# Kernel tuning notes

Measured on AMD Instinct MI355X. Metric: run time of the kernel, lower is better.

Reference implementation:

```python
import jax, jax.numpy as jnp
import numpy as np

N_HEAD = 16
DIM_K = 64
DIM_MODEL = N_HEAD * DIM_K  # 1024; seq_len is forced to equal dim_model by the reshape
SCALE = float(DIM_K ** 0.5)


def setup_inputs() -> dict:
    key = jax.random.key(0)
    ks = jax.random.split(key, 4)
    B, S, D = 32, DIM_MODEL, 1024
    x = jax.random.normal(ks[0], (B, S, D), dtype=jnp.float32)
    glorot = float(1.0 / np.sqrt(D))
    Wq = jax.random.normal(ks[1], (D, DIM_MODEL), dtype=jnp.float32) * glorot
    Wk = jax.random.normal(ks[2], (D, DIM_MODEL), dtype=jnp.float32) * glorot
    Wv = jax.random.normal(ks[3], (D, DIM_MODEL), dtype=jnp.float32) * glorot
    bq = jnp.zeros((DIM_MODEL,), jnp.float32)
    bk = jnp.zeros((DIM_MODEL,), jnp.float32)
    bv = jnp.zeros((DIM_MODEL,), jnp.float32)
    return {"x": x, "Wq": Wq, "bq": bq, "Wk": Wk, "bk": bk, "Wv": Wv, "bv": bv}


def reference(x, Wq, bq, Wk, bk, Wv, bv):
    # x: [B, S, D] with S == DIM_MODEL (required by the original reshape)
    B = x.shape[0]
    q = x @ Wq + bq  # [B, S, dm]
    k = x @ Wk + bk
    v = x @ Wv + bv
    # TF1 K.batch_dot(q, k, axes=[-1,-1]) -> tf.matmul(q, k, adjoint_a=True):
    # contracts over the SEQUENCE axis -> [B, dm, dm]
    y = jnp.einsum('bsd,bse->bde', q, k) / SCALE
    # softmax over dim_k-sized chunks of the last axis
    y = y.reshape(B, DIM_MODEL, N_HEAD, DIM_K)
    y = jax.nn.softmax(y, axis=-1)
    y = y.reshape(B, DIM_MODEL, DIM_MODEL)
    # TF1 K.batch_dot(v, y, axes=[2,3]) -> tf.matmul(v, y) (no adjoints)
    out = jnp.einsum('bsd,bde->bse', v, y)  # [B, S, dm]
    return out
```

## Files before the change

### kernel.cpp

```cpp
#include <hip/hip_runtime.h>
#include <hip/hip_bf16.h>

#define DM 1024
#define NB 32

typedef __bf16 bf16_t;
typedef __attribute__((ext_vector_type(8))) __bf16 bf16x8;
typedef __attribute__((ext_vector_type(4))) float  f32x4;

typedef __attribute__((address_space(1))) void gas_void;
typedef __attribute__((address_space(3))) void las_void;

__device__ __forceinline__ void async_lds16(const bf16_t* g, bf16_t* l) {
    __builtin_amdgcn_global_load_lds((gas_void*)g, (las_void*)l, 16, 0, 0);
}

__device__ inline float bf2f(bf16_t v) {
    union { unsigned short s; __bf16 b; } u; u.b = v;
    union { unsigned int i; float f; } w; w.i = ((unsigned int)u.s) << 16;
    return w.f;
}
__device__ inline bf16_t f2bf(float f) {
    union { unsigned int i; float f; } w; w.f = f;
    unsigned int r = (w.i + 0x7FFFu + ((w.i >> 16) & 1u)) >> 16;
    union { unsigned short s; __bf16 b; } u; u.s = (unsigned short)r;
    return u.b;
}

enum EpiMode { EPI_NONE = 0, EPI_BIAS_ROW = 1, EPI_BIAS_COL = 2, EPI_SCALE = 3 };

__global__ void detect_mode(const unsigned short* __restrict__ x, int* __restrict__ mode)
{
    if (threadIdx.x == 0 && blockIdx.x == 0) {
        int hits = 0;
        for (int i = 0; i < 2048; ++i) {
            unsigned e = (x[i] >> 7) & 0xFFu;
            hits += (e >= 0x8Du) ? 1 : 0;
        }
        *mode = (hits >= 16) ? 1 : 0;
    }
}

__global__ void convert_x(const void* __restrict__ xin, bf16_t* __restrict__ xb,
                          const int* __restrict__ modep, long long off, long long n8)
{
    const long long i = (long long)blockIdx.x * blockDim.x + threadIdx.x;
    if (i >= n8) return;
    bf16x8 o;
    if (*modep) {
        const float* s = (const float*)xin + off + i * 8;
#pragma unroll
        for (int j = 0; j < 8; ++j) o[j] = f2bf(s[j]);
    } else {
        o = *(const bf16x8*)((const bf16_t*)xin + off + i * 8);
    }
    *(bf16x8*)(xb + i * 8) = o;
}

__global__ void transpose3(const void* __restrict__ Wq, const void* __restrict__ Wk,
                           const void* __restrict__ Wv, bf16_t* __restrict__ Wt,
                           const int* __restrict__ modep)
{
    const int md = *modep;
    const void* src = (blockIdx.z == 0) ? Wq : (blockIdx.z == 1) ? Wk : Wv;
    bf16_t* dst = Wt + (size_t)blockIdx.z * DM * DM;
    __shared__ bf16_t T[64][72];
    const int tid = threadIdx.x;
    const int r  = tid >> 2;
    const int cp = tid & 3;
    const int r0 = blockIdx.y * 64;
    const int c0 = blockIdx.x * 64;
    const size_t base = (size_t)(r0 + r) * DM + c0 + cp * 16;
    bf16_t tmp[16];
    if (md) {
        const float* s = (const float*)src + base;
#pragma unroll
        for (int j = 0; j < 16; ++j) tmp[j] = f2bf(s[j]);
    } else {
        const bf16_t* s = (const bf16_t*)src + base;
        bf16x8 a = *(const bf16x8*)s;
        bf16x8 b = *(const bf16x8*)(s + 8);
#pragma unroll
        for (int j = 0; j < 8; ++j) { tmp[j] = a[j]; tmp[8 + j] = b[j]; }
    }
#pragma unroll
    for (int j = 0; j < 16; ++j) T[cp * 16 + j][r] = tmp[j];
    __syncthreads();
    bf16_t* d = dst + (size_t)(c0 + r) * DM + r0 + cp * 16;
    bf16x8 w0, w1;
#pragma unroll
    for (int j = 0; j < 8; ++j) w0[j] = T[r][cp * 16 + j];
#pragma unroll
    for (int j = 0; j < 8; ++j) w1[j] = T[r][cp * 16 + 8 + j];
    *(bf16x8*)d = w0;
    *(bf16x8*)(d + 8) = w1;
}

template <int MODE, bool DUALOUT>
__global__ __launch_bounds__(512, 2)
void gemm_nt8(const bf16_t* __restrict__ A, long long sA,
              const bf16_t* __restrict__ B, long long sB,
              void* __restrict__ C, long long sC, long long cOff,
              const void* __restrict__ bias, const int* __restrict__ modep,
              float scale)
{
    constexpr int K = 1024;
    constexpr int NT = K / 64;
    extern __shared__ bf16_t L[];

    int bx, by, z;
    {
        const int nwg  = 16 * (int)gridDim.z;
        const int orig = (int)blockIdx.x + 4 * ((int)blockIdx.y + 4 * (int)blockIdx.z);
        const int nid  = (orig & 7) * (nwg >> 3) + (orig >> 3);
        bx = nid & 3; by = (nid >> 2) & 3; z = nid >> 4;
    }

    const bf16_t* Ab = A + (size_t)z * (size_t)sA;
    const bf16_t* Bb = B + (size_t)z * (size_t)sB;
    const int gm0 = by * 256, gn0 = bx * 256;

    const int tid  = threadIdx.x;
    const int lane = tid & 63;
    const int w    = tid >> 6;
    const int rb   = w >> 1;
    const int cb   = w & 1;
    const int lm   = lane & 15;
    const int kg   = lane >> 4;

    f32x4 acc[4][2][4];
#pragma unroll
    for (int p = 0; p < 4; ++p)
#pragma unroll
        for (int i = 0; i < 2; ++i)
#pragma unroll
            for (int j = 0; j < 4; ++j) acc[p][i][j] = (f32x4)0.0f;

    auto stage = [&](int kt, int s, int b) {
        const bf16_t* P  = (s == 0 || s == 3) ? Ab : Bb;
        const int     g0 = (s == 0 || s == 3) ? gm0 : gn0;
        const int     h  = (s >= 2) ? 1 : 0;
        bf16_t* dst = L + (b * 4 + s) * 8192;
#pragma unroll
        for (int i = 0; i < 2; ++i) {
            const int ci  = i * 512 + tid;
            const int row = ci >> 3;
            const int kc  = (ci & 7) ^ (row & 7);
            async_lds16(P + (size_t)(g0 + h * 128 + row) * K + kt * 64 + kc * 8,
                        dst + ci * 8);
        }
    };

    auto rdfrag = [&](int b, int s, int r, int kc) -> bf16x8 {
        const int byte = r * 128 + ((kc ^ (r & 7)) * 16);
        return *(const bf16x8*)((const char*)(L + (b * 4 + s) * 8192) + byte);
    };

#pragma unroll
    for (int s = 0; s < 4; ++s) stage(0, s, 0);
    asm volatile("s_waitcnt vmcnt(2)" ::: "memory");
    __builtin_amdgcn_s_barrier();

#pragma unroll 1
    for (int kt = 0; kt < NT; ++kt) {
        const int cur = kt & 1;
        const int nkt = (kt + 1 < NT) ? kt + 1 : 0;
#pragma unroll
        for (int p = 0; p < 4; ++p) {
            const int sA_ = (p >> 1) ? 3 : 0;
            const int sB_ = (p & 1) ? 2 : 1;
            bf16x8 af[2][2], bg[4][2];
#pragma unroll
            for (int mt = 0; mt < 2; ++mt)
#pragma unroll
                for (int kk = 0; kk < 2; ++kk)
                    af[mt][kk] = rdfrag(cur, sA_, rb * 32 + mt * 16 + lm, kk * 4 + kg);
#pragma unroll
            for (int nt = 0; nt < 4; ++nt)
#pragma unroll
                for (int kk = 0; kk < 2; ++kk)
                    bg[nt][kk] = rdfrag(cur, sB_, cb * 64 + nt * 16 + lm, kk * 4 + kg);
            stage(nkt, p, cur ^ 1);
            __builtin_amdgcn_s_barrier();
            asm volatile("s_waitcnt lgkmcnt(0)" ::: "memory");
            __builtin_amdgcn_sched_barrier(0);
            __builtin_amdgcn_s_setprio(1);
#pragma unroll
            for (int kk = 0; kk < 2; ++kk)
#pragma unroll
                for (int mt = 0; mt < 2; ++mt)
#pragma unroll
                    for (int nt = 0; nt < 4; ++nt)
                        acc[p][mt][nt] = __builtin_amdgcn_mfma_f32_16x16x32_bf16(
                            af[mt][kk], bg[nt][kk], acc[p][mt][nt], 0, 0, 0);
            __builtin_amdgcn_s_setprio(0);
            if (p == 1) { asm volatile("s_waitcnt vmcnt(4)" ::: "memory"); }
            if (p == 3) { asm volatile("s_waitcnt vmcnt(2)" ::: "memory"); }
            __builtin_amdgcn_s_barrier();
        }
    }

    const int md = *modep;
#pragma unroll
    for (int p = 0; p < 4; ++p) {
        const int rbase = gm0 + (p >> 1) * 128 + rb * 32;
        const int cbase = gn0 + (p & 1) * 128 + cb * 64;
#pragma unroll
        for (int mt = 0; mt < 2; ++mt) {
            float rbias[4];
            if (MODE == EPI_BIAS_ROW) {
#pragma unroll
                for (int r = 0; r < 4; ++r) {
                    const int i = rbase + mt * 16 + kg * 4 + r;
                    rbias[r] = md ? ((const float*)bias)[i] : bf2f(((const bf16_t*)bias)[i]);
                }
            }
#pragma unroll
            for (int nt = 0; nt < 4; ++nt) {
                const int col = cbase + nt * 16 + lm;
                float cbias = 0.f;
                if (MODE == EPI_BIAS_COL)
                    cbias = md ? ((const float*)bias)[col] : bf2f(((const bf16_t*)bias)[col]);
#pragma unroll
                for (int r = 0; r < 4; ++r) {
                    const int row = rbase + mt * 16 + kg * 4 + r;
                    float vv = acc[p][mt][nt][r];
                    if (MODE == EPI_BIAS_ROW) vv += rbias[r];
                    if (MODE == EPI_BIAS_COL) vv += cbias;
                    if (MODE == EPI_SCALE)    vv *= scale;
                    const size_t off = (size_t)cOff + (size_t)z * sC + (size_t)row * 1024 + col;
                    if (DUALOUT && md) ((float*)C)[off] = vv;
                    else               ((bf16_t*)C)[off] = f2bf(vv);
                }
            }
        }
    }
}

__global__ void softmax_t_inplace(bf16_t* __restrict__ Y)
{
    const int b = blockIdx.z;
    int idx = blockIdx.x;
    int I = 0;
    while (idx >= 16 - I) { idx -= 16 - I; ++I; }
    const int J = I + idx;

    const int tid = threadIdx.x;
    const int r  = tid >> 2;
    const int cp = tid & 3;

    bf16_t* base = Y + ((size_t)b << 20);
    bf16_t* t0 = base + (size_t)(I * 64 + r) * DM + J * 64 + cp * 16;
    bf16_t* t1 = base + (size_t)(J * 64 + r) * DM + I * 64 + cp * 16;

    __shared__ bf16_t P0[64][72];
    __shared__ bf16_t P1[64][72];

    bf16x8 a0 = *(const bf16x8*)t0;
    bf16x8 a1 = *(const bf16x8*)(t0 + 8);
    bf16x8 c0v, c1v;
    if (J != I) { c0v = *(const bf16x8*)t1; c1v = *(const bf16x8*)(t1 + 8); }

    {
        float f[16];
#pragma unroll
        for (int j = 0; j < 8; ++j) f[j] = bf2f(a0[j]);
#pragma unroll
        for (int j = 0; j < 8; ++j) f[8 + j] = bf2f(a1[j]);
        float m = -1e30f;
#pragma unroll
        for (int j = 0; j < 16; ++j) m = fmaxf(m, f[j]);
        m = fmaxf(m, __shfl_xor(m, 1));
        m = fmaxf(m, __shfl_xor(m, 2));
        float s = 0.f;
#pragma unroll
        for (int j = 0; j < 16; ++j) { f[j] = __expf(f[j] - m); s += f[j]; }
        s += __shfl_xor(s, 1);
        s += __shfl_xor(s, 2);
        const float inv = 1.0f / s;
#pragma unroll
        for (int j = 0; j < 16; ++j) P0[cp * 16 + j][r] = f2bf(f[j] * inv);
    }
    if (J != I) {
        float f[16];
#pragma unroll
        for (int j = 0; j < 8; ++j) f[j] = bf2f(c0v[j]);
#pragma unroll
        for (int j = 0; j < 8; ++j) f[8 + j] = bf2f(c1v[j]);
        float m = -1e30f;
#pragma unroll
        for (int j = 0; j < 16; ++j) m = fmaxf(m, f[j]);
        m = fmaxf(m, __shfl_xor(m, 1));
        m = fmaxf(m, __shfl_xor(m, 2));
        float s = 0.f;
#pragma unroll
        for (int j = 0; j < 16; ++j) { f[j] = __expf(f[j] - m); s += f[j]; }
        s += __shfl_xor(s, 1);
        s += __shfl_xor(s, 2);
        const float inv = 1.0f / s;
#pragma unroll
        for (int j = 0; j < 16; ++j) P1[cp * 16 + j][r] = f2bf(f[j] * inv);
    }
    __syncthreads();

    bf16x8 w0, w1;
#pragma unroll
    for (int j = 0; j < 8; ++j) w0[j] = P0[r][cp * 16 + j];
#pragma unroll
    for (int j = 0; j < 8; ++j) w1[j] = P0[r][cp * 16 + 8 + j];
    *(bf16x8*)t1 = w0;
    *(bf16x8*)(t1 + 8) = w1;
    if (J != I) {
#pragma unroll
        for (int j = 0; j < 8; ++j) w0[j] = P1[r][cp * 16 + j];
#pragma unroll
        for (int j = 0; j < 8; ++j) w1[j] = P1[r][cp * 16 + 8 + j];
        *(bf16x8*)t0 = w0;
        *(bf16x8*)(t0 + 8) = w1;
    }
}

extern "C" void kernel_launch(void* const* d_in, const int* in_sizes, int n_in,
                              void* d_out, int out_size, void* d_ws, size_t ws_size,
                              hipStream_t stream)
{
    const void* x  = d_in[0];
    const void* Wq = d_in[1];
    const void* bq = d_in[2];
    const void* Wk = d_in[3];
    const void* bk = d_in[4];
    const void* Wv = d_in[5];
    const void* bv = d_in[6];

    static bool attr_done = false;
    if (!attr_done) {
        hipFuncSetAttribute((const void*)gemm_nt8<EPI_BIAS_ROW, false>,
                            hipFuncAttributeMaxDynamicSharedMemorySize, 131072);
        hipFuncSetAttribute((const void*)gemm_nt8<EPI_BIAS_COL, false>,
                            hipFuncAttributeMaxDynamicSharedMemorySize, 131072);
        hipFuncSetAttribute((const void*)gemm_nt8<EPI_SCALE, false>,
                            hipFuncAttributeMaxDynamicSharedMemorySize, 131072);
        hipFuncSetAttribute((const void*)gemm_nt8<EPI_NONE, true>,
                            hipFuncAttributeMaxDynamicSharedMemorySize, 131072);
        attr_done = true;
    }

    char* ws = (char*)d_ws;
    int* mode = (int*)ws;
    const size_t MB2 = (size_t)DM * DM * 2;
    const size_t hdr = 256;
    int CB = NB;
    while (CB > 1 && hdr + 3 * MB2 + 4 * (size_t)CB * MB2 > ws_size) CB >>= 1;

    bf16_t* Wt = (bf16_t*)(ws + hdr);
    bf16_t* xb = (bf16_t*)(ws + hdr + 3 * MB2);
    bf16_t* qt = xb + (size_t)CB * DM * DM;
    bf16_t* kt = qt + (size_t)CB * DM * DM;
    bf16_t* y  = kt + (size_t)CB * DM * DM;
    bf16_t* v  = qt;

    detect_mode<<<1, 64, 0, stream>>>((const unsigned short*)x, mode);
    transpose3<<<dim3(16, 16, 3), 256, 0, stream>>>(Wq, Wk, Wv, Wt, mode);

    const long long msz = (long long)DM * DM;
    for (int c = 0; c < NB; c += CB) {
        const int zb = (NB - c < CB) ? (NB - c) : CB;
        const long long n8 = (long long)zb * msz / 8;
        convert_x<<<(int)((n8 + 255) / 256), 256, 0, stream>>>(x, xb, mode, (long long)c * msz, n8);

        const dim3 g8(4, 4, zb), blk8(512);
        gemm_nt8<EPI_BIAS_ROW, false><<<g8, blk8, 131072, stream>>>(Wt, 0, xb, msz, qt, msz, 0, bq, mode, 1.f);
        gemm_nt8<EPI_BIAS_ROW, false><<<g8, blk8, 131072, stream>>>(Wt + msz, 0, xb, msz, kt, msz, 0, bk, mode, 1.f);
        gemm_nt8<EPI_SCALE, false><<<g8, blk8, 131072, stream>>>(qt, msz, kt, msz, y, msz, 0, nullptr, mode, 0.125f);
        softmax_t_inplace<<<dim3(136, 1, zb), 256, 0, stream>>>(y);
        gemm_nt8<EPI_BIAS_COL, false><<<g8, blk8, 131072, stream>>>(xb, msz, Wt + 2 * msz, 0, v, msz, 0, bv, mode, 1.f);
        gemm_nt8<EPI_NONE, true><<<g8, blk8, 131072, stream>>>(v, msz, y, msz, d_out, msz, (long long)c * msz, nullptr, mode, 1.f);
    }
}
```

Before: 698.7 us.

## Software-pipeline LDS fragment reads with double-buffered registers across MFMA phases

Restructures the GEMM main loop so LDS fragment reads for the next phase are issued before the current phase's MFMAs, using two register sets for the A and B fragments. The stage layout is reordered so A and B halves alternate, and phase order changes so fragments are reused across two consecutive phases. Barriers and vmcnt waits are rearranged to match. The goal is to hide LDS latency behind matrix math, at the cost of more VGPRs and a more fragile wait/barrier schedule.

Result: faster. 671.2 us (-3.9%).

```diff
diff --git a/kernel.cpp b/kernel.cpp
--- a/kernel.cpp
+++ b/kernel.cpp
@@ -136,9 +136,11 @@
 #pragma unroll
             for (int j = 0; j < 4; ++j) acc[p][i][j] = (f32x4)0.0f;
 
+    bf16x8 af0[2][2], af1[2][2], bg0[4][2], bg1[4][2];
+
     auto stage = [&](int kt, int s, int b) {
-        const bf16_t* P  = (s == 0 || s == 3) ? Ab : Bb;
-        const int     g0 = (s == 0 || s == 3) ? gm0 : gn0;
+        const bf16_t* P  = (s & 1) ? Bb : Ab;
+        const int     g0 = (s & 1) ? gn0 : gm0;
         const int     h  = (s >= 2) ? 1 : 0;
         bf16_t* dst = L + (b * 4 + s) * 8192;
 #pragma unroll
@@ -155,56 +157,86 @@
         const int byte = r * 128 + ((kc ^ (r & 7)) * 16);
         return *(const bf16x8*)((const char*)(L + (b * 4 + s) * 8192) + byte);
     };
+    auto rdA = [&](int b, int s, bf16x8 (&dst)[2][2]) {
+#pragma unroll
+        for (int mt = 0; mt < 2; ++mt)
+#pragma unroll
+            for (int kk = 0; kk < 2; ++kk)
+                dst[mt][kk] = rdfrag(b, s, rb * 32 + mt * 16 + lm, kk * 4 + kg);
+    };
+    auto rdB = [&](int b, int s, bf16x8 (&dst)[4][2]) {
+#pragma unroll
+        for (int nt = 0; nt < 4; ++nt)
+#pragma unroll
+            for (int kk = 0; kk < 2; ++kk)
+                dst[nt][kk] = rdfrag(b, s, cb * 64 + nt * 16 + lm, kk * 4 + kg);
+    };
+
+#define MFMA_PHASE(P, AF, BG)                                                  \
+    __builtin_amdgcn_s_setprio(1);                                             \
+    _Pragma("unroll")                                                          \
+    for (int kk = 0; kk < 2; ++kk)                                             \
+        _Pragma("unroll")                                                      \
+        for (int mt = 0; mt < 2; ++mt)                                         \
+            _Pragma("unroll")                                                  \
+            for (int nt = 0; nt < 4; ++nt)                                     \
+                acc[P][mt][nt] = __builtin_amdgcn_mfma_f32_16x16x32_bf16(      \
+                    AF[mt][kk], BG[nt][kk], acc[P][mt][nt], 0, 0, 0);          \
+    __builtin_amdgcn_s_setprio(0);
 
 #pragma unroll
     for (int s = 0; s < 4; ++s) stage(0, s, 0);
+    asm volatile("s_waitcnt vmcnt(4)" ::: "memory");
+    __builtin_amdgcn_s_barrier();
+    rdA(0, 0, af0);
+    rdB(0, 1, bg0);
     asm volatile("s_waitcnt vmcnt(2)" ::: "memory");
     __builtin_amdgcn_s_barrier();
 
 #pragma unroll 1
     for (int kt = 0; kt < NT; ++kt) {
         const int cur = kt & 1;
+        const int nxt = cur ^ 1;
         const int nkt = (kt + 1 < NT) ? kt + 1 : 0;
-#pragma unroll
-        for (int p = 0; p < 4; ++p) {
-            const int sA_ = (p >> 1) ? 3 : 0;
-            const int sB_ = (p & 1) ? 2 : 1;
-            bf16x8 af[2][2], bg[4][2];
-#pragma unroll
-            for (int mt = 0; mt < 2; ++mt)
-#pragma unroll
-                for (int kk = 0; kk < 2; ++kk)
-                    af[mt][kk] = rdfrag(cur, sA_, rb * 32 + mt * 16 + lm, kk * 4 + kg);
-#pragma unroll
-            for (int nt = 0; nt < 4; ++nt)
-#pragma unroll
-                for (int kk = 0; kk < 2; ++kk)
-                    bg[nt][kk] = rdfrag(cur, sB_, cb * 64 + nt * 16 + lm, kk * 4 + kg);
-            stage(nkt, p, cur ^ 1);
-            __builtin_amdgcn_s_barrier();
-            asm volatile("s_waitcnt lgkmcnt(0)" ::: "memory");
-            __builtin_amdgcn_sched_barrier(0);
-            __builtin_amdgcn_s_setprio(1);
-#pragma unroll
-            for (int kk = 0; kk < 2; ++kk)
-#pragma unroll
-                for (int mt = 0; mt < 2; ++mt)
-#pragma unroll
-                    for (int nt = 0; nt < 4; ++nt)
-                        acc[p][mt][nt] = __builtin_amdgcn_mfma_f32_16x16x32_bf16(
-                            af[mt][kk], bg[nt][kk], acc[p][mt][nt], 0, 0, 0);
-            __builtin_amdgcn_s_setprio(0);
-            if (p == 1) { asm volatile("s_waitcnt vmcnt(4)" ::: "memory"); }
-            if (p == 3) { asm volatile("s_waitcnt vmcnt(2)" ::: "memory"); }
-            __builtin_amdgcn_s_barrier();
-        }
-    }
+
+        rdA(cur, 2, af1);
+        stage(nkt, 0, nxt);
+        __builtin_amdgcn_sched_barrier(0);
+        MFMA_PHASE(0, af0, bg0)
+        __builtin_amdgcn_sched_barrier(0);
+        asm volatile("s_waitcnt vmcnt(2)" ::: "memory");
+        __builtin_amdgcn_s_barrier();
+
+        rdB(cur, 3, bg1);
+        stage(nkt, 1, nxt);
+        __builtin_amdgcn_sched_barrier(0);
+        MFMA_PHASE(1, af1, bg0)
+        __builtin_amdgcn_sched_barrier(0);
+        __builtin_amdgcn_s_barrier();
+
+        stage(nkt, 2, nxt);
+        __builtin_amdgcn_sched_barrier(0);
+        MFMA_PHASE(2, af0, bg1)
+        __builtin_amdgcn_sched_barrier(0);
+        asm volatile("s_waitcnt vmcnt(2)" ::: "memory");
+        __builtin_amdgcn_s_barrier();
+
+        rdA(nxt, 0, af0);
+        rdB(nxt, 1, bg0);
+        stage(nkt, 3, nxt);
+        __builtin_amdgcn_sched_barrier(0);
+        MFMA_PHASE(3, af1, bg1)
+        __builtin_amdgcn_sched_barrier(0);
+        asm volatile("s_waitcnt vmcnt(2)" ::: "memory");
+        __builtin_amdgcn_s_barrier();
+    }
+#undef MFMA_PHASE
 
     const int md = *modep;
 #pragma unroll
     for (int p = 0; p < 4; ++p) {
-        const int rbase = gm0 + (p >> 1) * 128 + rb * 32;
-        const int cbase = gn0 + (p & 1) * 128 + cb * 64;
+        const int rbase = gm0 + (p & 1) * 128 + rb * 32;
+        const int cbase = gn0 + (p >> 1) * 128 + cb * 64;
 #pragma unroll
         for (int mt = 0; mt < 2; ++mt) {
             float rbias[4];
```
